# Kernel tuning notes

Measured on AMD Instinct MI355X. Metric: run time of the kernel, lower is better.

Reference implementation:

```python
import jax, jax.numpy as jnp
from jax import lax
import numpy as np

DIM = 64
NUM_HEADS = 1
HEAD_DIM = DIM // NUM_HEADS
SR = 8
EPS = 1e-5


def setup_inputs() -> dict:
    key = jax.random.key(0)
    ks = jax.random.split(key, 12)
    B, H, W = 8, 128, 128
    N = H * W
    s = 1.0 / np.sqrt(DIM)
    x = jax.random.normal(ks[0], (B, N, DIM), dtype=jnp.float32)
    Wq = jax.random.normal(ks[1], (DIM, DIM), dtype=jnp.float32) * s
    bq = jnp.zeros((DIM,), jnp.float32)
    Wk = jax.random.normal(ks[2], (DIM, DIM), dtype=jnp.float32) * s
    bk = jnp.zeros((DIM,), jnp.float32)
    Wv = jax.random.normal(ks[3], (DIM, DIM), dtype=jnp.float32) * s
    bv = jnp.zeros((DIM,), jnp.float32)
    # Conv2D kernel in HWIO layout (Keras default), kernel=stride=SR, padding VALID
    Wsr = jax.random.normal(ks[4], (SR, SR, DIM, DIM), dtype=jnp.float32) * (1.0 / np.sqrt(SR * SR * DIM))
    bsr = jnp.zeros((DIM,), jnp.float32)
    gamma = jnp.ones((DIM,), jnp.float32)
    beta = jnp.zeros((DIM,), jnp.float32)
    Wp = jax.random.normal(ks[5], (DIM, DIM), dtype=jnp.float32) * s
    bp = jnp.zeros((DIM,), jnp.float32)
    return {"x": x, "Wq": Wq, "bq": bq, "Wk": Wk, "bk": bk, "Wv": Wv, "bv": bv,
            "Wsr": Wsr, "bsr": bsr, "gamma": gamma, "beta": beta, "Wp": Wp, "bp": bp,
            "H": H, "W": W}


def reference(x, Wq, bq, Wk, bk, Wv, bv, Wsr, bsr, gamma, beta, Wp, bp, H, W):
    B, N, C = x.shape
    # queries: [B, heads, N, head_dim]
    q = (x @ Wq + bq).reshape(B, N, NUM_HEADS, HEAD_DIM).transpose(0, 2, 1, 3)
    # spatial reduction: strided conv over the token grid, then LayerNorm
    xs = x.reshape(B, H, W, C)
    xs = lax.conv_general_dilated(xs, Wsr, window_strides=(SR, SR), padding='VALID',
                                  dimension_numbers=('NHWC', 'HWIO', 'NHWC')) + bsr
    xs = xs.reshape(B, -1, C)  # [B, Nkv, C], Nkv = (H//SR)*(W//SR)
    mu = jnp.mean(xs, axis=-1, keepdims=True)
    var = jnp.var(xs, axis=-1, keepdims=True)
    xs = (xs - mu) * lax.rsqrt(var + EPS) * gamma + beta
    k = (xs @ Wk + bk).reshape(B, -1, NUM_HEADS, HEAD_DIM).transpose(0, 2, 1, 3)
    v = (xs @ Wv + bv).reshape(B, -1, NUM_HEADS, HEAD_DIM).transpose(0, 2, 1, 3)
    scale = jnp.asarray(np.sqrt(HEAD_DIM), x.dtype)
    attn = jnp.einsum('bhqd,bhkd->bhqk', q, k) / scale
    attn = jax.nn.softmax(attn, axis=-1)
    out = jnp.einsum('bhqk,bhkd->bhqd', attn, v)
    out = out.transpose(0, 2, 1, 3).reshape(B, N, NUM_HEADS * HEAD_DIM)
    return out @ Wp + bp
```

## Files before the change

kernel.cpp:

```cpp
#include <hip/hip_runtime.h>

typedef unsigned short u16;
typedef short short8 __attribute__((ext_vector_type(8)));
typedef short short4v __attribute__((ext_vector_type(4)));
typedef float f32x4 __attribute__((ext_vector_type(4)));
typedef float f4 __attribute__((ext_vector_type(4)));

#define MFMA16(a, b, c) __builtin_amdgcn_mfma_f32_16x16x32_bf16(a, b, c, 0, 0, 0)
#define MFMA1K(a, b, c) __builtin_amdgcn_mfma_f32_16x16x16bf16_1k(a, b, c, 0, 0, 0)

__device__ inline u16 f2bf(float f) {
    unsigned int v = __builtin_bit_cast(unsigned int, f);
    unsigned int r = (v + 0x7FFFu + ((v >> 16) & 1u)) >> 16;
    return (u16)r;
}
__device__ inline short4v pack4(f4 v) {
    short4v r;
#pragma unroll
    for (int j = 0; j < 4; ++j) r[j] = (short)f2bf(v[j]);
    return r;
}

__global__ __launch_bounds__(256) void prep_kernel(
    const float* __restrict__ Wsr, const float* __restrict__ Wq,
    const float* __restrict__ Wp,
    u16* __restrict__ WsrT, u16* __restrict__ WqT, u16* __restrict__ WpT)
{
    const int bid = blockIdx.x;
    const int tid = threadIdx.x;
    __shared__ float sT[64 * 65];
    const float* src;
    u16* dst;
    if (bid < 64)      { src = Wsr + (size_t)bid * 4096; dst = WsrT + (size_t)bid * 4096; }
    else if (bid == 64){ src = Wq;  dst = WqT; }
    else               { src = Wp;  dst = WpT; }
#pragma unroll
    for (int p = 0; p < 4; ++p) {
        int idx = p * 256 + tid;
        int r = idx >> 4, c4 = (idx & 15) * 4;
        f4 v = *(const f4*)(src + r * 64 + c4);
#pragma unroll
        for (int j = 0; j < 4; ++j) sT[r * 65 + c4 + j] = v[j];
    }
    __syncthreads();
#pragma unroll
    for (int p = 0; p < 2; ++p) {
        int idx = p * 256 + tid;
        int co = idx >> 3, g = (idx & 7) * 8;
        short8 o;
#pragma unroll
        for (int j = 0; j < 8; ++j) o[j] = (short)f2bf(sT[(g + j) * 65 + co]);
        *(short8*)(dst + (size_t)co * 64 + g) = o;
    }
}

__global__ __launch_bounds__(256) void conv_partial_kernel(
    const float* __restrict__ x, const u16* __restrict__ WsrT,
    float* __restrict__ partials)
{
    const int mtile  = blockIdx.x & 31;
    const int ksplit = blockIdx.x >> 5;
    const int tid  = threadIdx.x;
    const int wave = tid >> 6;
    const int lane = tid & 63;
    const int l15  = lane & 15;
    const int quad = lane >> 4;

    __shared__ u16 sA[4][64 * 72];
    __shared__ u16 sB[4][64 * 72];

    const int token0 = mtile * 64;

#pragma unroll
    for (int chunk = 0; chunk < 4; ++chunk) {
        const int cell = ksplit * 4 + chunk;
        const int py = cell >> 3, px = cell & 7;
#pragma unroll
        for (int p = 0; p < 4; ++p) {
            int idx = p * 256 + tid;
            int r = idx >> 4, c4 = (idx & 15) * 4;
            int token = token0 + r;
            int b = token >> 8, rm = token & 255;
            int oy = rm >> 4, ox = rm & 15;
            int y = oy * 8 + py, xc = ox * 8 + px;
            f4 xv = *(const f4*)(x + ((size_t)(b * 16384 + y * 128 + xc)) * 64 + c4);
            short4v s;
#pragma unroll
            for (int j = 0; j < 4; ++j) s[j] = (short)f2bf(xv[j]);
            *(short4v*)&sA[chunk][r * 72 + c4] = s;
        }
#pragma unroll
        for (int p = 0; p < 2; ++p) {
            int idx = p * 256 + tid;
            int co = idx >> 3, g = (idx & 7) * 8;
            *(short8*)&sB[chunk][co * 72 + g] =
                *(const short8*)(WsrT + (size_t)cell * 4096 + co * 64 + g);
        }
    }
    __syncthreads();

    f32x4 acc[4];
#pragma unroll
    for (int nt = 0; nt < 4; ++nt) { acc[nt][0]=0.f; acc[nt][1]=0.f; acc[nt][2]=0.f; acc[nt][3]=0.f; }

#pragma unroll
    for (int chunk = 0; chunk < 4; ++chunk) {
#pragma unroll
        for (int ks = 0; ks < 2; ++ks) {
            short8 af = *(const short8*)&sA[chunk][(wave * 16 + l15) * 72 + ks * 32 + quad * 8];
#pragma unroll
            for (int nt = 0; nt < 4; ++nt) {
                short8 bf = *(const short8*)&sB[chunk][(nt * 16 + l15) * 72 + ks * 32 + quad * 8];
                acc[nt] = MFMA16(af, bf, acc[nt]);
            }
        }
    }
    float* outp = partials + (size_t)ksplit * 131072;
#pragma unroll
    for (int nt = 0; nt < 4; ++nt)
#pragma unroll
        for (int i = 0; i < 4; ++i) {
            int row = token0 + wave * 16 + quad * 4 + i;
            outp[(size_t)row * 64 + nt * 16 + l15] = acc[nt][i];
        }
}

__global__ __launch_bounds__(256) void lnkv_kernel(
    const float* __restrict__ partials, const float* __restrict__ bsr,
    const float* __restrict__ gamma, const float* __restrict__ beta,
    const float* __restrict__ Wk, const float* __restrict__ bk,
    const float* __restrict__ Wv, const float* __restrict__ bv,
    u16* __restrict__ kbuf, u16* __restrict__ vTbuf)
{
    const int wave = threadIdx.x >> 6;
    const int c    = threadIdx.x & 63;
    const int token = blockIdx.x * 4 + wave;

    float acc = 0.f;
#pragma unroll
    for (int s = 0; s < 16; ++s)
        acc += partials[(size_t)s * 131072 + (size_t)token * 64 + c];
    acc += bsr[c];

    float sum = acc, sumsq = acc * acc;
#pragma unroll
    for (int m = 1; m < 64; m <<= 1) {
        sum   += __shfl_xor(sum, m, 64);
        sumsq += __shfl_xor(sumsq, m, 64);
    }
    float mean = sum * (1.f / 64.f);
    float var  = sumsq * (1.f / 64.f) - mean * mean;
    float inv  = rsqrtf(var + 1e-5f);
    float xn   = (acc - mean) * inv * gamma[c] + beta[c];

    __shared__ float sxn[4][64];
    sxn[wave][c] = xn;

    float ka = bk[c], va = bv[c];
#pragma unroll 8
    for (int ci = 0; ci < 64; ++ci) {
        float xv = sxn[wave][ci];
        ka += xv * Wk[ci * 64 + c];
        va += xv * Wv[ci * 64 + c];
    }
    kbuf[(size_t)token * 64 + c] = f2bf(ka);
    int b = token >> 8, t = token & 255;
    vTbuf[(size_t)b * 16384 + c * 256 + t] = f2bf(va);
}

__global__ __launch_bounds__(512) void attn_kernel(
    const float* __restrict__ x, const u16* __restrict__ WqT,
    const float* __restrict__ bq, const u16* __restrict__ WpT,
    const float* __restrict__ bp, const u16* __restrict__ kbuf,
    const u16* __restrict__ vTbuf, float* __restrict__ out)
{
    const int batch = blockIdx.x >> 6;
    const int row0  = (blockIdx.x & 63) * 256;
    const int tid  = threadIdx.x;
    const int wave = tid >> 6;
    const int lane = tid & 63;
    const int l15  = lane & 15;
    const int quad = lane >> 4;

    __shared__ u16 sK[256 * 72];
    __shared__ u16 sV[64 * 264];
    __shared__ u16 sWq[64 * 72];
    __shared__ u16 sWp[64 * 72];

    const int qbase = row0 + wave * 32;

    f4 xq[4][2];
#pragma unroll
    for (int kt = 0; kt < 4; ++kt)
#pragma unroll
        for (int qt = 0; qt < 2; ++qt)
            xq[kt][qt] = *(const f4*)(x + ((size_t)(batch * 16384 + qbase + qt * 16 + l15)) * 64 + kt * 16 + quad * 4);

#pragma unroll
    for (int p = 0; p < 4; ++p) {
        int idx = p * 512 + tid; int tt = idx >> 3, seg = idx & 7;
        *(short8*)&sK[tt * 72 + seg * 8] =
            *(const short8*)(kbuf + ((size_t)(batch * 256 + tt)) * 64 + seg * 8);
    }
#pragma unroll
    for (int p = 0; p < 4; ++p) {
        int idx = p * 512 + tid; int d = idx >> 5, seg = idx & 31;
        *(short8*)&sV[d * 264 + seg * 8] =
            *(const short8*)(vTbuf + ((size_t)(batch * 64 + d)) * 256 + seg * 8);
    }
    {
        int co = tid >> 3, g = (tid & 7) * 8;
        *(short8*)&sWq[co * 72 + g] = *(const short8*)(WqT + (size_t)co * 64 + g);
        *(short8*)&sWp[co * 72 + g] = *(const short8*)(WpT + (size_t)co * 64 + g);
    }
    __syncthreads();

    f32x4 qT[2][4];
#pragma unroll
    for (int qt = 0; qt < 2; ++qt)
#pragma unroll
        for (int ct = 0; ct < 4; ++ct) { qT[qt][ct][0]=0.f; qT[qt][ct][1]=0.f; qT[qt][ct][2]=0.f; qT[qt][ct][3]=0.f; }
#pragma unroll
    for (int kt = 0; kt < 4; ++kt) {
        short4v bfr[2];
#pragma unroll
        for (int qt = 0; qt < 2; ++qt) bfr[qt] = pack4(xq[kt][qt]);
#pragma unroll
        for (int ct = 0; ct < 4; ++ct) {
            short4v a = *(const short4v*)&sWq[(ct * 16 + l15) * 72 + kt * 16 + quad * 4];
#pragma unroll
            for (int qt = 0; qt < 2; ++qt) qT[qt][ct] = MFMA1K(a, bfr[qt], qT[qt][ct]);
        }
    }
    short4v qf[2][4];
#pragma unroll
    for (int ct = 0; ct < 4; ++ct) {
        f4 bqv = *(const f4*)(bq + ct * 16 + quad * 4);
#pragma unroll
        for (int qt = 0; qt < 2; ++qt) {
            f4 t;
#pragma unroll
            for (int i = 0; i < 4; ++i) t[i] = (qT[qt][ct][i] + bqv[i]) * 0.125f;
            qf[qt][ct] = pack4(t);
        }
    }

    f32x4 st[2][16];
#pragma unroll
    for (int qt = 0; qt < 2; ++qt)
#pragma unroll
        for (int mt = 0; mt < 16; ++mt) { st[qt][mt][0]=0.f; st[qt][mt][1]=0.f; st[qt][mt][2]=0.f; st[qt][mt][3]=0.f; }
#pragma unroll
    for (int mt = 0; mt < 16; ++mt)
#pragma unroll
        for (int kt = 0; kt < 4; ++kt) {
            short4v a = *(const short4v*)&sK[(mt * 16 + l15) * 72 + kt * 16 + quad * 4];
#pragma unroll
            for (int qt = 0; qt < 2; ++qt) st[qt][mt] = MFMA1K(a, qf[qt][kt], st[qt][mt]);
        }

    short4v pf[2][16];
    float linv[2];
#pragma unroll
    for (int qt = 0; qt < 2; ++qt) {
        float mx = -1e30f;
#pragma unroll
        for (int mt = 0; mt < 16; ++mt)
#pragma unroll
            for (int i = 0; i < 4; ++i) mx = fmaxf(mx, st[qt][mt][i]);
        mx = fmaxf(mx, __shfl_xor(mx, 16, 64));
        mx = fmaxf(mx, __shfl_xor(mx, 32, 64));
        float l = 0.f;
#pragma unroll
        for (int mt = 0; mt < 16; ++mt) {
            f4 e;
#pragma unroll
            for (int i = 0; i < 4; ++i) { e[i] = __expf(st[qt][mt][i] - mx); l += e[i]; }
            pf[qt][mt] = pack4(e);
        }
        l += __shfl_xor(l, 16, 64);
        l += __shfl_xor(l, 32, 64);
        linv[qt] = 1.0f / l;
    }

    f32x4 ot[2][4];
#pragma unroll
    for (int qt = 0; qt < 2; ++qt)
#pragma unroll
        for (int dt = 0; dt < 4; ++dt) { ot[qt][dt][0]=0.f; ot[qt][dt][1]=0.f; ot[qt][dt][2]=0.f; ot[qt][dt][3]=0.f; }
#pragma unroll
    for (int mt = 0; mt < 16; ++mt)
#pragma unroll
        for (int dt = 0; dt < 4; ++dt) {
            short4v a = *(const short4v*)&sV[(dt * 16 + l15) * 264 + mt * 16 + quad * 4];
#pragma unroll
            for (int qt = 0; qt < 2; ++qt) ot[qt][dt] = MFMA1K(a, pf[qt][mt], ot[qt][dt]);
        }

    short4v of[2][4];
#pragma unroll
    for (int dt = 0; dt < 4; ++dt)
#pragma unroll
        for (int qt = 0; qt < 2; ++qt) {
            f4 t;
#pragma unroll
            for (int i = 0; i < 4; ++i) t[i] = ot[qt][dt][i] * linv[qt];
            of[qt][dt] = pack4(t);
        }
    f32x4 ft[2][4];
#pragma unroll
    for (int qt = 0; qt < 2; ++qt)
#pragma unroll
        for (int ct = 0; ct < 4; ++ct) { ft[qt][ct][0]=0.f; ft[qt][ct][1]=0.f; ft[qt][ct][2]=0.f; ft[qt][ct][3]=0.f; }
#pragma unroll
    for (int kt = 0; kt < 4; ++kt)
#pragma unroll
        for (int ct = 0; ct < 4; ++ct) {
            short4v a = *(const short4v*)&sWp[(ct * 16 + l15) * 72 + kt * 16 + quad * 4];
#pragma unroll
            for (int qt = 0; qt < 2; ++qt) ft[qt][ct] = MFMA1K(a, of[qt][kt], ft[qt][ct]);
        }

#pragma unroll
    for (int ct = 0; ct < 4; ++ct) {
        f4 bpv = *(const f4*)(bp + ct * 16 + quad * 4);
#pragma unroll
        for (int qt = 0; qt < 2; ++qt) {
            f4 r;
#pragma unroll
            for (int i = 0; i < 4; ++i) r[i] = ft[qt][ct][i] + bpv[i];
            *(f4*)(out + ((size_t)(batch * 16384 + qbase + qt * 16 + l15)) * 64 + ct * 16 + quad * 4) = r;
        }
    }
}

extern "C" void kernel_launch(void* const* d_in, const int* in_sizes, int n_in,
                              void* d_out, int out_size, void* d_ws, size_t ws_size,
                              hipStream_t stream) {
    const float* x     = (const float*)d_in[0];
    const float* Wq    = (const float*)d_in[1];
    const float* bq    = (const float*)d_in[2];
    const float* Wk    = (const float*)d_in[3];
    const float* bk    = (const float*)d_in[4];
    const float* Wv    = (const float*)d_in[5];
    const float* bv    = (const float*)d_in[6];
    const float* Wsr   = (const float*)d_in[7];
    const float* bsr   = (const float*)d_in[8];
    const float* gamma = (const float*)d_in[9];
    const float* beta  = (const float*)d_in[10];
    const float* Wp    = (const float*)d_in[11];
    const float* bp    = (const float*)d_in[12];

    char* w = (char*)d_ws;
    float* partials = (float*)w;
    u16* kbuf  = (u16*)(w + 8388608);
    u16* vTbuf = (u16*)(w + 8388608 + 262144);
    u16* WsrT  = (u16*)(w + 8388608 + 524288);
    u16* WqT   = (u16*)(w + 8388608 + 524288 + 524288);
    u16* WpT   = (u16*)(w + 8388608 + 524288 + 524288 + 8192);
    float* out = (float*)d_out;

    prep_kernel<<<66, 256, 0, stream>>>(Wsr, Wq, Wp, WsrT, WqT, WpT);
    conv_partial_kernel<<<512, 256, 0, stream>>>(x, WsrT, partials);
    lnkv_kernel<<<512, 256, 0, stream>>>(partials, bsr, gamma, beta, Wk, bk, Wv, bv, kbuf, vTbuf);
    attn_kernel<<<512, 512, 0, stream>>>(x, WqT, bq, WpT, bp, kbuf, vTbuf, out);
}
```

Baseline: 144.9 us.

## Fuse LayerNorm and K/V projection into conv kernel via last-block atomic election

```diff
diff --git a/kernel.cpp b/kernel.cpp
--- a/kernel.cpp
+++ b/kernel.cpp
@@ -24,7 +24,8 @@
 __global__ __launch_bounds__(256) void prep_kernel(
     const float* __restrict__ Wsr, const float* __restrict__ Wq,
     const float* __restrict__ Wp,
-    u16* __restrict__ WsrT, u16* __restrict__ WqT, u16* __restrict__ WpT)
+    u16* __restrict__ WsrT, u16* __restrict__ WqT, u16* __restrict__ WpT,
+    int* __restrict__ counters)
 {
     const int bid = blockIdx.x;
     const int tid = threadIdx.x;
@@ -34,6 +35,7 @@
     if (bid < 64)      { src = Wsr + (size_t)bid * 4096; dst = WsrT + (size_t)bid * 4096; }
     else if (bid == 64){ src = Wq;  dst = WqT; }
     else               { src = Wp;  dst = WpT; }
+    if (bid == 65 && tid < 32) counters[tid] = 0;
 #pragma unroll
     for (int p = 0; p < 4; ++p) {
         int idx = p * 256 + tid;
@@ -56,7 +58,12 @@
 
 __global__ __launch_bounds__(256) void conv_partial_kernel(
     const float* __restrict__ x, const u16* __restrict__ WsrT,
-    float* __restrict__ partials)
+    float* __restrict__ partials, int* __restrict__ counters,
+    const float* __restrict__ bsr,
+    const float* __restrict__ gamma, const float* __restrict__ beta,
+    const float* __restrict__ Wk, const float* __restrict__ bk,
+    const float* __restrict__ Wv, const float* __restrict__ bv,
+    u16* __restrict__ kbuf, u16* __restrict__ vTbuf)
 {
     const int mtile  = blockIdx.x & 31;
     const int ksplit = blockIdx.x >> 5;
@@ -123,49 +130,47 @@
             int row = token0 + wave * 16 + quad * 4 + i;
             outp[(size_t)row * 64 + nt * 16 + l15] = acc[nt][i];
         }
-}
-
-__global__ __launch_bounds__(256) void lnkv_kernel(
-    const float* __restrict__ partials, const float* __restrict__ bsr,
-    const float* __restrict__ gamma, const float* __restrict__ beta,
-    const float* __restrict__ Wk, const float* __restrict__ bk,
-    const float* __restrict__ Wv, const float* __restrict__ bv,
-    u16* __restrict__ kbuf, u16* __restrict__ vTbuf)
-{
-    const int wave = threadIdx.x >> 6;
-    const int c    = threadIdx.x & 63;
-    const int token = blockIdx.x * 4 + wave;
-
-    float acc = 0.f;
-#pragma unroll
-    for (int s = 0; s < 16; ++s)
-        acc += partials[(size_t)s * 131072 + (size_t)token * 64 + c];
-    acc += bsr[c];
-
-    float sum = acc, sumsq = acc * acc;
-#pragma unroll
-    for (int m = 1; m < 64; m <<= 1) {
-        sum   += __shfl_xor(sum, m, 64);
-        sumsq += __shfl_xor(sumsq, m, 64);
-    }
-    float mean = sum * (1.f / 64.f);
-    float var  = sumsq * (1.f / 64.f) - mean * mean;
-    float inv  = rsqrtf(var + 1e-5f);
-    float xn   = (acc - mean) * inv * gamma[c] + beta[c];
-
+
+    __threadfence();
+    __shared__ int elect;
+    if (tid == 0) elect = (atomicAdd(&counters[mtile], 1) == 15) ? 1 : 0;
+    __syncthreads();
+    if (!elect) return;
+    __threadfence();
+
+    const int c = lane;
     __shared__ float sxn[4][64];
-    sxn[wave][c] = xn;
-
-    float ka = bk[c], va = bv[c];
+    for (int s = 0; s < 16; ++s) {
+        const int token = token0 + wave * 16 + s;
+        float a = 0.f;
+#pragma unroll
+        for (int p = 0; p < 16; ++p)
+            a += partials[(size_t)p * 131072 + (size_t)token * 64 + c];
+        a += bsr[c];
+
+        float sum = a, sumsq = a * a;
+#pragma unroll
+        for (int m = 1; m < 64; m <<= 1) {
+            sum   += __shfl_xor(sum, m, 64);
+            sumsq += __shfl_xor(sumsq, m, 64);
+        }
+        float mean = sum * (1.f / 64.f);
+        float var  = sumsq * (1.f / 64.f) - mean * mean;
+        float inv  = rsqrtf(var + 1e-5f);
+        float xn   = (a - mean) * inv * gamma[c] + beta[c];
+        sxn[wave][c] = xn;
+
+        float ka = bk[c], va = bv[c];
 #pragma unroll 8
-    for (int ci = 0; ci < 64; ++ci) {
-        float xv = sxn[wave][ci];
-        ka += xv * Wk[ci * 64 + c];
-        va += xv * Wv[ci * 64 + c];
-    }
-    kbuf[(size_t)token * 64 + c] = f2bf(ka);
-    int b = token >> 8, t = token & 255;
-    vTbuf[(size_t)b * 16384 + c * 256 + t] = f2bf(va);
+        for (int ci = 0; ci < 64; ++ci) {
+            float xv = sxn[wave][ci];
+            ka += xv * Wk[ci * 64 + c];
+            va += xv * Wv[ci * 64 + c];
+        }
+        kbuf[(size_t)token * 64 + c] = f2bf(ka);
+        int bb = token >> 8, tt = token & 255;
+        vTbuf[(size_t)bb * 16384 + c * 256 + tt] = f2bf(va);
+    }
 }
 
 __global__ __launch_bounds__(512) void attn_kernel(
@@ -357,11 +362,13 @@
     u16* vTbuf = (u16*)(w + 8388608 + 262144);
     u16* WsrT  = (u16*)(w + 8388608 + 524288);
     u16* WqT   = (u16*)(w + 8388608 + 524288 + 524288);
-    u16* WpT   = (u16*)(w + 8388608 + 524288 + 524288 + 8192);
+    u16* WpT   = (u16*)(w + 9445376);
+    int* counters = (int*)(w + 9453568);
     float* out = (float*)d_out;
 
-    prep_kernel<<<66, 256, 0, stream>>>(Wsr, Wq, Wp, WsrT, WqT, WpT);
-    conv_partial_kernel<<<512, 256, 0, stream>>>(x, WsrT, partials);
-    lnkv_kernel<<<512, 256, 0, stream>>>(partials, bsr, gamma, beta, Wk, bk, Wv, bv, kbuf, vTbuf);
+    prep_kernel<<<66, 256, 0, stream>>>(Wsr, Wq, Wp, WsrT, WqT, WpT, counters);
+    conv_partial_kernel<<<512, 256, 0, stream>>>(x, WsrT, partials, counters,
+                                                 bsr, gamma, beta, Wk, bk, Wv, bv,
+                                                 kbuf, vTbuf);
     attn_kernel<<<512, 512, 0, stream>>>(x, WqT, bq, WpT, bp, kbuf, vTbuf, out);
 }
```

Measured after the change: 236.2 us. 63.0% more time.
